# Optimization experiments

Measured on AMD Instinct MI355X. Metric: run time of the kernel, lower is better.

## Reference

```python
import jax, jax.numpy as jnp
import numpy as np

B, T, C, H, O = 64, 256, 2048, 512, 11
THRESHOLD = 1.0
LEAK = 0.003
OUTPUT_LEAK = LEAK * 0.5


def setup_inputs() -> dict:
    key = jax.random.key(0)
    k1, k2, k3, k4 = jax.random.split(key, 4)
    x = jax.random.normal(k1, (B, T, C), dtype=jnp.float32)
    # xavier_uniform(gain=0.1) for fc1: bound = 0.1*sqrt(6/(C+H))
    b1 = 0.1 * np.sqrt(6.0 / (C + H))
    w1 = jax.random.uniform(k2, (H, C), jnp.float32, -b1, b1)
    # orthogonal(gain=0.1) for fc_rec -> approximate with small gaussian scaled like orthogonal rows
    w_rec = 0.1 * jnp.linalg.qr(jax.random.normal(k3, (H, H), jnp.float32))[0]
    b2 = 0.3 * np.sqrt(6.0 / (H + O))
    w2 = jax.random.uniform(k4, (O, H), jnp.float32, -b2, b2)
    return {"x": x, "w1": w1, "w_rec": w_rec, "w2": w2}


def reference(x, w1, w_rec, w2):
    batch, t_steps, _ = x.shape
    n_hidden = w1.shape[0]
    n_output = w2.shape[0]
    dt = x.dtype

    def step(carry, x_t):
        v1, spk1, v2, out_sum = carry
        # input + recurrent current: [B,H]
        i1 = x_t @ w1.T + spk1 @ w_rec.T
        # subtractive LIF: leak, threshold, subtractive reset
        v1 = v1 + i1 - LEAK
        spk = (v1 >= THRESHOLD).astype(dt)
        v1 = v1 - spk * THRESHOLD
        # non-spiking output accumulator neuron: [B,O]
        i2 = spk @ w2.T
        v2 = jnp.maximum(v2 + i2 - OUTPUT_LEAK, 0.0)
        out_sum = out_sum + v2
        return (v1, spk, v2, out_sum), None

    init = (
        jnp.zeros((batch, n_hidden), dt),
        jnp.zeros((batch, n_hidden), dt),
        jnp.zeros((batch, n_output), dt),
        jnp.zeros((batch, n_output), dt),
    )
    (_, _, _, out_sum), _ = jax.lax.scan(step, init, jnp.swapaxes(x, 0, 1))
    return out_sum / t_steps
```

## Files before the change

kernel.cpp:

```cpp
#include <hip/hip_runtime.h>
#include <cstddef>

#define B_ 64
#define T_ 256
#define C_ 2048
#define H_ 512
#define O_ 11
#define THRESH 1.0f
#define LEAK_ 0.003f
#define OLEAK_ 0.0015f

typedef float v2f __attribute__((ext_vector_type(2)));

__global__ __launch_bounds__(256) void transpose_wrec(const float* __restrict__ w,
                                                      float* __restrict__ wt) {
    __shared__ float tile[32][33];
    int tx = threadIdx.x, ty = threadIdx.y;
    int x = blockIdx.x * 32 + tx;
    int y = blockIdx.y * 32 + ty;
#pragma unroll
    for (int i = 0; i < 32; i += 8)
        tile[ty + i][tx] = w[(size_t)(y + i) * H_ + x];
    __syncthreads();
    int x2 = blockIdx.y * 32 + tx;
    int y2 = blockIdx.x * 32 + ty;
#pragma unroll
    for (int i = 0; i < 32; i += 8)
        wt[(size_t)(y2 + i) * H_ + x2] = tile[tx][ty + i];
}

#define BM 128
#define BN 128
#define BK 16

template <int S>
__global__ __launch_bounds__(256) void gemm_ff(const float* __restrict__ A,
                                               const float* __restrict__ Bw,
                                               float* __restrict__ Pout) {
    const int K = C_;
    const int N = H_;
    const int kLen  = C_ / S;
    const int kBase = blockIdx.z * kLen;

    __shared__ float As[BK][BM];
    __shared__ float Bs[BK][BN];

    const int t  = threadIdx.x;
    const int tx = t & 15;
    const int ty = t >> 4;
    const int lr = t >> 2;
    const int lc = (t & 3) * 4;

    const float* Aptr = A  + (size_t)(blockIdx.y * BM + lr) * K + kBase + lc;
    const float* Bptr = Bw + (size_t)(blockIdx.x * BN + lr) * K + kBase + lc;

    v2f acc[8][4];
#pragma unroll
    for (int i = 0; i < 8; ++i)
#pragma unroll
        for (int j = 0; j < 4; ++j) acc[i][j] = (v2f){0.f, 0.f};

    for (int k0 = 0; k0 < kLen; k0 += BK) {
        float4 a0 = *(const float4*)(Aptr);
        float4 a1 = *(const float4*)(Aptr + (size_t)64 * K);
        float4 b0 = *(const float4*)(Bptr);
        float4 b1 = *(const float4*)(Bptr + (size_t)64 * K);
        Aptr += BK; Bptr += BK;

        __syncthreads();
        As[lc + 0][lr] = a0.x; As[lc + 1][lr] = a0.y;
        As[lc + 2][lr] = a0.z; As[lc + 3][lr] = a0.w;
        As[lc + 0][lr + 64] = a1.x; As[lc + 1][lr + 64] = a1.y;
        As[lc + 2][lr + 64] = a1.z; As[lc + 3][lr + 64] = a1.w;
        Bs[lc + 0][lr] = b0.x; Bs[lc + 1][lr] = b0.y;
        Bs[lc + 2][lr] = b0.z; Bs[lc + 3][lr] = b0.w;
        Bs[lc + 0][lr + 64] = b1.x; Bs[lc + 1][lr + 64] = b1.y;
        Bs[lc + 2][lr + 64] = b1.z; Bs[lc + 3][lr + 64] = b1.w;
        __syncthreads();

#pragma unroll
        for (int k = 0; k < BK; ++k) {
            float4 alo = *(const float4*)&As[k][ty * 4];
            float4 ahi = *(const float4*)&As[k][64 + ty * 4];
            float4 blo = *(const float4*)&Bs[k][tx * 4];
            float4 bhi = *(const float4*)&Bs[k][64 + tx * 4];
            v2f b0v = {blo.x, blo.y}, b1v = {blo.z, blo.w};
            v2f b2v = {bhi.x, bhi.y}, b3v = {bhi.z, bhi.w};
            float av[8] = {alo.x, alo.y, alo.z, alo.w, ahi.x, ahi.y, ahi.z, ahi.w};
#pragma unroll
            for (int i = 0; i < 8; ++i) {
                v2f ai = {av[i], av[i]};
                acc[i][0] += ai * b0v;
                acc[i][1] += ai * b1v;
                acc[i][2] += ai * b2v;
                acc[i][3] += ai * b3v;
            }
        }
    }

    float* P = Pout + (size_t)blockIdx.z * ((size_t)B_ * T_ * H_);
#pragma unroll
    for (int i = 0; i < 8; ++i) {
        int row = blockIdx.y * BM + (i < 4 ? ty * 4 + i : 64 + ty * 4 + (i - 4));
        float* Cp = P + (size_t)row * N + blockIdx.x * BN;
        float4 c0 = {acc[i][0].x, acc[i][0].y, acc[i][1].x, acc[i][1].y};
        float4 c1 = {acc[i][2].x, acc[i][2].y, acc[i][3].x, acc[i][3].y};
        *(float4*)(Cp + tx * 4)      = c0;
        *(float4*)(Cp + 64 + tx * 4) = c1;
    }
}

template <int S>
__global__ __launch_bounds__(512) void snn_rec(const float* __restrict__ I1,
                                               const float* __restrict__ wrT,
                                               const float* __restrict__ w2,
                                               float* __restrict__ out) {
    const int b    = blockIdx.x;
    const int h    = threadIdx.x;
    const int lane = h & 63;
    const int w    = h >> 6;

    __shared__ float w2sT[H_ * 12];
    __shared__ int   lists[2][H_];
    __shared__ int   wcnt[8];
    __shared__ float v2s[O_];
    __shared__ float osum[O_];

    for (int k = h; k < H_; k += H_) {}
#pragma unroll
    for (int o = 0; o < O_; ++o) w2sT[h * 12 + o] = w2[o * H_ + h];
    if (h < O_) { v2s[h] = 0.f; osum[h] = 0.f; }

    float v1 = 0.f;
    int   pc = 0;
    const float*  i1p  = I1 + (size_t)b * T_ * H_ + h;
    const float*  wr_h = wrT + h;
    const size_t  PARTF = (size_t)B_ * T_ * H_;

    float pf[S];
#pragma unroll
    for (int s = 0; s < S; ++s) pf[s] = i1p[s * PARTF];
    __syncthreads();

    for (int t = 0; t < T_; ++t) {
        const int cur = t & 1;

        float acc = -LEAK_;
#pragma unroll
        for (int s = 0; s < S; ++s) acc += pf[s];

        const int tn = (t + 1 < T_) ? t + 1 : t;
#pragma unroll
        for (int s = 0; s < S; ++s) pf[s] = i1p[s * PARTF + (size_t)tn * H_];

        const int* pl = lists[cur ^ 1];
        int j = 0;
        for (; j + 7 < pc; j += 8) {
            const int4 ia = *(const int4*)(pl + j);
            const int4 ib = *(const int4*)(pl + j + 4);
            float g0 = wr_h[ia.x * H_];
            float g1 = wr_h[ia.y * H_];
            float g2 = wr_h[ia.z * H_];
            float g3 = wr_h[ia.w * H_];
            float g4 = wr_h[ib.x * H_];
            float g5 = wr_h[ib.y * H_];
            float g6 = wr_h[ib.z * H_];
            float g7 = wr_h[ib.w * H_];
            acc += g0; acc += g1; acc += g2; acc += g3;
            acc += g4; acc += g5; acc += g6; acc += g7;
        }
        for (; j < pc; ++j) acc += wr_h[pl[j] * H_];

        v1 += acc;
        const bool spike = (v1 >= THRESH);
        if (spike) v1 -= THRESH;

        unsigned long long m = __ballot(spike);
        int lb = __popcll(m & ((1ull << lane) - 1ull));
        if (lane == 0) wcnt[w] = (int)__popcll(m);
        __syncthreads();

        int base = 0, tot = 0;
#pragma unroll
        for (int ww = 0; ww < 8; ++ww) {
            int c = wcnt[ww];
            if (ww < w) base += c;
            tot += c;
        }
        if (spike) lists[cur][base + lb] = h;
        __syncthreads();

        if (h < O_) {
            const int* cl = lists[cur];
            float s = 0.f;
            for (int j2 = 0; j2 < tot; ++j2) s += w2sT[cl[j2] * 12 + h];
            float v2 = v2s[h] + s - OLEAK_;
            v2 = v2 > 0.f ? v2 : 0.f;
            v2s[h] = v2;
            osum[h] += v2;
        }
        pc = tot;
    }
    __syncthreads();
    if (h < O_) out[b * O_ + h] = osum[h] * (1.0f / (float)T_);
}

extern "C" void kernel_launch(void* const* d_in, const int* in_sizes, int n_in,
                              void* d_out, int out_size, void* d_ws, size_t ws_size,
                              hipStream_t stream) {
    const float* x     = (const float*)d_in[0];
    const float* w1    = (const float*)d_in[1];
    const float* w_rec = (const float*)d_in[2];
    const float* w2    = (const float*)d_in[3];
    float* out = (float*)d_out;

    const size_t PART = (size_t)B_ * T_ * H_ * sizeof(float);
    const size_t WRT  = (size_t)H_ * H_ * sizeof(float);

    int S = 1;
    if (ws_size >= 4 * PART + WRT) S = 4;
    else if (ws_size >= 2 * PART + WRT) S = 2;

    float* P   = (float*)d_ws;
    float* wrT = (float*)((char*)d_ws + (size_t)S * PART);

    transpose_wrec<<<dim3(H_ / 32, H_ / 32), dim3(32, 8), 0, stream>>>(w_rec, wrT);

    dim3 ggrid(H_ / BN, (B_ * T_) / BM, S);
    switch (S) {
        case 4:
            gemm_ff<4><<<ggrid, dim3(256), 0, stream>>>(x, w1, P);
            snn_rec<4><<<dim3(B_), dim3(H_), 0, stream>>>(P, wrT, w2, out);
            break;
        case 2:
            gemm_ff<2><<<ggrid, dim3(256), 0, stream>>>(x, w1, P);
            snn_rec<2><<<dim3(B_), dim3(H_), 0, stream>>>(P, wrT, w2, out);
            break;
        default:
            gemm_ff<1><<<ggrid, dim3(256), 0, stream>>>(x, w1, P);
            snn_rec<1><<<dim3(B_), dim3(H_), 0, stream>>>(P, wrT, w2, out);
            break;
    }
}
```

Baseline: 764.3 us.

## Enlarge GEMM per-thread tile with register prefetch; use spike bitmasks in recurrence

The feed-forward GEMM drops to 128 threads, each computing an 8x16 output tile. Global loads for the next K-slice are issued into registers before the current slice is computed, shared tiles are padded, and results go out through nontemporal stores. The recurrent kernel replaces the prefix-sum spike list, and one of its barriers, with per-wave ballot bitmasks in shared memory. It also keeps output-neuron state in registers and double-buffers the input-current prefetch two steps ahead. The larger per-thread tile raises register pressure and can lower occupancy, and the bitmask scan turns sequential ctz walks into serial work per wave.

```diff
diff --git a/kernel.cpp b/kernel.cpp
--- a/kernel.cpp
+++ b/kernel.cpp
@@ -11,6 +11,7 @@
 #define OLEAK_ 0.0015f
 
 typedef float v2f __attribute__((ext_vector_type(2)));
+typedef float v4f __attribute__((ext_vector_type(4)));
 
 __global__ __launch_bounds__(256) void transpose_wrec(const float* __restrict__ w,
                                                       float* __restrict__ wt) {
@@ -32,81 +33,96 @@
 #define BM 128
 #define BN 128
 #define BK 16
+#define LDA (BM + 4)
+#define LDB (BN + 4)
 
 template <int S>
-__global__ __launch_bounds__(256) void gemm_ff(const float* __restrict__ A,
-                                               const float* __restrict__ Bw,
-                                               float* __restrict__ Pout) {
+__global__ __launch_bounds__(128, 2) void gemm_ff(const float* __restrict__ A,
+                                                  const float* __restrict__ Bw,
+                                                  float* __restrict__ Pout) {
     const int K = C_;
     const int N = H_;
     const int kLen  = C_ / S;
     const int kBase = blockIdx.z * kLen;
 
-    __shared__ float As[BK][BM];
-    __shared__ float Bs[BK][BN];
+    __shared__ float As[BK][LDA];
+    __shared__ float Bs[BK][LDB];
 
     const int t  = threadIdx.x;
-    const int tx = t & 15;
-    const int ty = t >> 4;
+    const int tx = t & 7;
+    const int ty = t >> 3;
     const int lr = t >> 2;
     const int lc = (t & 3) * 4;
 
-    const float* Aptr = A  + (size_t)(blockIdx.y * BM + lr) * K + kBase + lc;
-    const float* Bptr = Bw + (size_t)(blockIdx.x * BN + lr) * K + kBase + lc;
-
-    v2f acc[8][4];
+    const float* Ap = A  + (size_t)(blockIdx.y * BM + lr) * K + kBase + lc;
+    const float* Bp = Bw + (size_t)(blockIdx.x * BN + lr) * K + kBase + lc;
+
+    v2f acc[8][8];
 #pragma unroll
     for (int i = 0; i < 8; ++i)
 #pragma unroll
-        for (int j = 0; j < 4; ++j) acc[i][j] = (v2f){0.f, 0.f};
-
-    for (int k0 = 0; k0 < kLen; k0 += BK) {
-        float4 a0 = *(const float4*)(Aptr);
-        float4 a1 = *(const float4*)(Aptr + (size_t)64 * K);
-        float4 b0 = *(const float4*)(Bptr);
-        float4 b1 = *(const float4*)(Bptr + (size_t)64 * K);
-        Aptr += BK; Bptr += BK;
-
+        for (int j = 0; j < 8; ++j) acc[i][j] = (v2f){0.f, 0.f};
+
+    float4 ra[4], rb[4];
+#pragma unroll
+    for (int q = 0; q < 4; ++q) ra[q] = *(const float4*)(Ap + (size_t)(32 * q) * K);
+#pragma unroll
+    for (int q = 0; q < 4; ++q) rb[q] = *(const float4*)(Bp + (size_t)(32 * q) * K);
+
+    for (int k0 = 0;;) {
         __syncthreads();
-        As[lc + 0][lr] = a0.x; As[lc + 1][lr] = a0.y;
-        As[lc + 2][lr] = a0.z; As[lc + 3][lr] = a0.w;
-        As[lc + 0][lr + 64] = a1.x; As[lc + 1][lr + 64] = a1.y;
-        As[lc + 2][lr + 64] = a1.z; As[lc + 3][lr + 64] = a1.w;
-        Bs[lc + 0][lr] = b0.x; Bs[lc + 1][lr] = b0.y;
-        Bs[lc + 2][lr] = b0.z; Bs[lc + 3][lr] = b0.w;
-        Bs[lc + 0][lr + 64] = b1.x; Bs[lc + 1][lr + 64] = b1.y;
-        Bs[lc + 2][lr + 64] = b1.z; Bs[lc + 3][lr + 64] = b1.w;
+#pragma unroll
+        for (int q = 0; q < 4; ++q) {
+            const int r = lr + 32 * q;
+            As[lc + 0][r] = ra[q].x; As[lc + 1][r] = ra[q].y;
+            As[lc + 2][r] = ra[q].z; As[lc + 3][r] = ra[q].w;
+            Bs[lc + 0][r] = rb[q].x; Bs[lc + 1][r] = rb[q].y;
+            Bs[lc + 2][r] = rb[q].z; Bs[lc + 3][r] = rb[q].w;
+        }
         __syncthreads();
 
+        k0 += BK;
+        const bool more = (k0 < kLen);
+        if (more) {
+            Ap += BK; Bp += BK;
+#pragma unroll
+            for (int q = 0; q < 4; ++q) ra[q] = *(const float4*)(Ap + (size_t)(32 * q) * K);
+#pragma unroll
+            for (int q = 0; q < 4; ++q) rb[q] = *(const float4*)(Bp + (size_t)(32 * q) * K);
+        }
+
 #pragma unroll
         for (int k = 0; k < BK; ++k) {
-            float4 alo = *(const float4*)&As[k][ty * 4];
-            float4 ahi = *(const float4*)&As[k][64 + ty * 4];
-            float4 blo = *(const float4*)&Bs[k][tx * 4];
-            float4 bhi = *(const float4*)&Bs[k][64 + tx * 4];
-            v2f b0v = {blo.x, blo.y}, b1v = {blo.z, blo.w};
-            v2f b2v = {bhi.x, bhi.y}, b3v = {bhi.z, bhi.w};
-            float av[8] = {alo.x, alo.y, alo.z, alo.w, ahi.x, ahi.y, ahi.z, ahi.w};
+            float4 a0 = *(const float4*)&As[k][ty * 8];
+            float4 a1 = *(const float4*)&As[k][ty * 8 + 4];
+            float4 b0 = *(const float4*)&Bs[k][tx * 4];
+            float4 b1 = *(const float4*)&Bs[k][32 + tx * 4];
+            float4 b2 = *(const float4*)&Bs[k][64 + tx * 4];
+            float4 b3 = *(const float4*)&Bs[k][96 + tx * 4];
+            v2f bv[8] = {{b0.x, b0.y}, {b0.z, b0.w}, {b1.x, b1.y}, {b1.z, b1.w},
+                         {b2.x, b2.y}, {b2.z, b2.w}, {b3.x, b3.y}, {b3.z, b3.w}};
+            float av[8] = {a0.x, a0.y, a0.z, a0.w, a1.x, a1.y, a1.z, a1.w};
 #pragma unroll
             for (int i = 0; i < 8; ++i) {
                 v2f ai = {av[i], av[i]};
-                acc[i][0] += ai * b0v;
-                acc[i][1] += ai * b1v;
-                acc[i][2] += ai * b2v;
-                acc[i][3] += ai * b3v;
+#pragma unroll
+                for (int j = 0; j < 8; ++j) acc[i][j] += ai * bv[j];
             }
         }
+        if (!more) break;
     }
 
     float* P = Pout + (size_t)blockIdx.z * ((size_t)B_ * T_ * H_);
 #pragma unroll
     for (int i = 0; i < 8; ++i) {
-        int row = blockIdx.y * BM + (i < 4 ? ty * 4 + i : 64 + ty * 4 + (i - 4));
+        const int row = blockIdx.y * BM + ty * 8 + i;
         float* Cp = P + (size_t)row * N + blockIdx.x * BN;
-        float4 c0 = {acc[i][0].x, acc[i][0].y, acc[i][1].x, acc[i][1].y};
-        float4 c1 = {acc[i][2].x, acc[i][2].y, acc[i][3].x, acc[i][3].y};
-        *(float4*)(Cp + tx * 4)      = c0;
-        *(float4*)(Cp + 64 + tx * 4) = c1;
+#pragma unroll
+        for (int s = 0; s < 4; ++s) {
+            v4f c = {acc[i][2 * s].x, acc[i][2 * s].y,
+                     acc[i][2 * s + 1].x, acc[i][2 * s + 1].y};
+            __builtin_nontemporal_store(c, (v4f*)(Cp + s * 32 + tx * 4));
+        }
     }
 }
 
@@ -121,88 +137,82 @@
     const int w    = h >> 6;
 
     __shared__ float w2sT[H_ * 12];
-    __shared__ int   lists[2][H_];
-    __shared__ int   wcnt[8];
-    __shared__ float v2s[O_];
-    __shared__ float osum[O_];
-
-    for (int k = h; k < H_; k += H_) {}
+    __shared__ unsigned long long masks[2][8];
+
 #pragma unroll
     for (int o = 0; o < O_; ++o) w2sT[h * 12 + o] = w2[o * H_ + h];
-    if (h < O_) { v2s[h] = 0.f; osum[h] = 0.f; }
+    if (h < 8) { masks[0][h] = 0ull; masks[1][h] = 0ull; }
 
     float v1 = 0.f;
-    int   pc = 0;
+    float v2 = 0.f;
+    float osum = 0.f;
+
     const float*  i1p  = I1 + (size_t)b * T_ * H_ + h;
     const float*  wr_h = wrT + h;
     const size_t  PARTF = (size_t)B_ * T_ * H_;
 
-    float pf[S];
-#pragma unroll
-    for (int s = 0; s < S; ++s) pf[s] = i1p[s * PARTF];
+    float pfA[S], pfB[S];
+#pragma unroll
+    for (int s = 0; s < S; ++s) pfA[s] = __builtin_nontemporal_load(i1p + s * PARTF);
+#pragma unroll
+    for (int s = 0; s < S; ++s) pfB[s] = __builtin_nontemporal_load(i1p + s * PARTF + H_);
     __syncthreads();
 
     for (int t = 0; t < T_; ++t) {
         const int cur = t & 1;
 
         float acc = -LEAK_;
-#pragma unroll
-        for (int s = 0; s < S; ++s) acc += pf[s];
-
-        const int tn = (t + 1 < T_) ? t + 1 : t;
-#pragma unroll
-        for (int s = 0; s < S; ++s) pf[s] = i1p[s * PARTF + (size_t)tn * H_];
-
-        const int* pl = lists[cur ^ 1];
-        int j = 0;
-        for (; j + 7 < pc; j += 8) {
-            const int4 ia = *(const int4*)(pl + j);
-            const int4 ib = *(const int4*)(pl + j + 4);
-            float g0 = wr_h[ia.x * H_];
-            float g1 = wr_h[ia.y * H_];
-            float g2 = wr_h[ia.z * H_];
-            float g3 = wr_h[ia.w * H_];
-            float g4 = wr_h[ib.x * H_];
-            float g5 = wr_h[ib.y * H_];
-            float g6 = wr_h[ib.z * H_];
-            float g7 = wr_h[ib.w * H_];
-            acc += g0; acc += g1; acc += g2; acc += g3;
-            acc += g4; acc += g5; acc += g6; acc += g7;
-        }
-        for (; j < pc; ++j) acc += wr_h[pl[j] * H_];
+        if (cur == 0) {
+#pragma unroll
+            for (int s = 0; s < S; ++s) acc += pfA[s];
+            const size_t tn = (size_t)((t + 2 < T_) ? t + 2 : t);
+#pragma unroll
+            for (int s = 0; s < S; ++s)
+                pfA[s] = __builtin_nontemporal_load(i1p + s * PARTF + tn * H_);
+        } else {
+#pragma unroll
+            for (int s = 0; s < S; ++s) acc += pfB[s];
+            const size_t tn = (size_t)((t + 2 < T_) ? t + 2 : t);
+#pragma unroll
+            for (int s = 0; s < S; ++s)
+                pfB[s] = __builtin_nontemporal_load(i1p + s * PARTF + tn * H_);
+        }
+
+#pragma unroll
+        for (int ww = 0; ww < 8; ++ww) {
+            unsigned long long m = masks[cur ^ 1][ww];
+            while (m) {
+                const int idx = (ww << 6) + __builtin_ctzll(m);
+                m &= m - 1;
+                acc += wr_h[idx * H_];
+            }
+        }
 
         v1 += acc;
         const bool spike = (v1 >= THRESH);
         if (spike) v1 -= THRESH;
 
-        unsigned long long m = __ballot(spike);
-        int lb = __popcll(m & ((1ull << lane) - 1ull));
-        if (lane == 0) wcnt[w] = (int)__popcll(m);
+        const unsigned long long bm = __ballot(spike);
+        if (lane == 0) masks[cur][w] = bm;
         __syncthreads();
 
-        int base = 0, tot = 0;
-#pragma unroll
-        for (int ww = 0; ww < 8; ++ww) {
-            int c = wcnt[ww];
-            if (ww < w) base += c;
-            tot += c;
-        }
-        if (spike) lists[cur][base + lb] = h;
-        __syncthreads();
-
         if (h < O_) {
-            const int* cl = lists[cur];
-            float s = 0.f;
-            for (int j2 = 0; j2 < tot; ++j2) s += w2sT[cl[j2] * 12 + h];
-            float v2 = v2s[h] + s - OLEAK_;
-            v2 = v2 > 0.f ? v2 : 0.f;
-            v2s[h] = v2;
-            osum[h] += v2;
-        }
-        pc = tot;
-    }
-    __syncthreads();
-    if (h < O_) out[b * O_ + h] = osum[h] * (1.0f / (float)T_);
+            float s2 = 0.f;
+#pragma unroll
+            for (int ww = 0; ww < 8; ++ww) {
+                unsigned long long m = masks[cur][ww];
+                while (m) {
+                    const int idx = (ww << 6) + __builtin_ctzll(m);
+                    m &= m - 1;
+                    s2 += w2sT[idx * 12 + h];
+                }
+            }
+            float nv2 = v2 + s2 - OLEAK_;
+            v2 = nv2 > 0.f ? nv2 : 0.f;
+            osum += v2;
+        }
+    }
+    if (h < O_) out[b * O_ + h] = osum * (1.0f / (float)T_);
 }
 
 extern "C" void kernel_launch(void* const* d_in, const int* in_sizes, int n_in,
@@ -229,15 +239,15 @@
     dim3 ggrid(H_ / BN, (B_ * T_) / BM, S);
     switch (S) {
         case 4:
-            gemm_ff<4><<<ggrid, dim3(256), 0, stream>>>(x, w1, P);
+            gemm_ff<4><<<ggrid, dim3(128), 0, stream>>>(x, w1, P);
             snn_rec<4><<<dim3(B_), dim3(H_), 0, stream>>>(P, wrT, w2, out);
             break;
         case 2:
-            gemm_ff<2><<<ggrid, dim3(256), 0, stream>>>(x, w1, P);
+            gemm_ff<2><<<ggrid, dim3(128), 0, stream>>>(x, w1, P);
             snn_rec<2><<<dim3(B_), dim3(H_), 0, stream>>>(P, wrT, w2, out);
             break;
         default:
-            gemm_ff<1><<<ggrid, dim3(256), 0, stream>>>(x, w1, P);
+            gemm_ff<1><<<ggrid, dim3(128), 0, stream>>>(x, w1, P);
             snn_rec<1><<<dim3(B_), dim3(H_), 0, stream>>>(P, wrT, w2, out);
             break;
     }
```

Measured after the change: 906.1 us. 1.19x slower.

## Prefetch GEMM tiles, swizzle block order, pad LDS, deepen SNN prefetch

Applied to the files above, without the earlier changes.

The GEMM now loads the next K-tile into registers while it computes the current one, remaps block indices into an XCD-aware order, pads the LDS tiles to avoid bank conflicts, and writes outputs with nontemporal stores. The recurrent kernel prefetches input currents two steps ahead with nontemporal loads and unrolls the sparse gather over the spike list by 16. Together these aim to hide global-memory latency in both stages and to improve cache use, at the cost of more registers. The swizzle assumes the grid size is 4x128xS.

```diff
diff --git a/kernel.cpp b/kernel.cpp
--- a/kernel.cpp
+++ b/kernel.cpp
@@ -11,6 +11,7 @@
 #define OLEAK_ 0.0015f
 
 typedef float v2f __attribute__((ext_vector_type(2)));
+typedef float v4f __attribute__((ext_vector_type(4)));
 
 __global__ __launch_bounds__(256) void transpose_wrec(const float* __restrict__ w,
                                                       float* __restrict__ wt) {
@@ -32,6 +33,7 @@
 #define BM 128
 #define BN 128
 #define BK 16
+#define LDT (BM + 4)
 
 template <int S>
 __global__ __launch_bounds__(256) void gemm_ff(const float* __restrict__ A,
@@ -39,11 +41,18 @@
                                                float* __restrict__ Pout) {
     const int K = C_;
     const int N = H_;
-    const int kLen  = C_ / S;
-    const int kBase = blockIdx.z * kLen;
-
-    __shared__ float As[BK][BM];
-    __shared__ float Bs[BK][BN];
+    const int kLen = C_ / S;
+
+    const int i  = blockIdx.x + 4 * blockIdx.y + 512 * blockIdx.z;
+    const int l  = (i & 7) * (64 * S) + (i >> 3);
+    const int bx = l & 3;
+    const int by = (l >> 2) & 127;
+    const int bz = l >> 9;
+
+    const int kBase = bz * kLen;
+
+    __shared__ float As[BK][LDT];
+    __shared__ float Bs[BK][LDT];
 
     const int t  = threadIdx.x;
     const int tx = t & 15;
@@ -51,22 +60,21 @@
     const int lr = t >> 2;
     const int lc = (t & 3) * 4;
 
-    const float* Aptr = A  + (size_t)(blockIdx.y * BM + lr) * K + kBase + lc;
-    const float* Bptr = Bw + (size_t)(blockIdx.x * BN + lr) * K + kBase + lc;
+    const float* Ap = A  + (size_t)(by * BM + lr) * K + kBase + lc;
+    const float* Bp = Bw + (size_t)(bx * BN + lr) * K + kBase + lc;
 
     v2f acc[8][4];
 #pragma unroll
-    for (int i = 0; i < 8; ++i)
-#pragma unroll
-        for (int j = 0; j < 4; ++j) acc[i][j] = (v2f){0.f, 0.f};
-
-    for (int k0 = 0; k0 < kLen; k0 += BK) {
-        float4 a0 = *(const float4*)(Aptr);
-        float4 a1 = *(const float4*)(Aptr + (size_t)64 * K);
-        float4 b0 = *(const float4*)(Bptr);
-        float4 b1 = *(const float4*)(Bptr + (size_t)64 * K);
-        Aptr += BK; Bptr += BK;
-
+    for (int ii = 0; ii < 8; ++ii)
+#pragma unroll
+        for (int j = 0; j < 4; ++j) acc[ii][j] = (v2f){0.f, 0.f};
+
+    float4 a0 = *(const float4*)(Ap);
+    float4 a1 = *(const float4*)(Ap + (size_t)64 * K);
+    float4 b0 = *(const float4*)(Bp);
+    float4 b1 = *(const float4*)(Bp + (size_t)64 * K);
+
+    for (int k0 = 0;;) {
         __syncthreads();
         As[lc + 0][lr] = a0.x; As[lc + 1][lr] = a0.y;
         As[lc + 2][lr] = a0.z; As[lc + 3][lr] = a0.w;
@@ -78,6 +86,16 @@
         Bs[lc + 2][lr + 64] = b1.z; Bs[lc + 3][lr + 64] = b1.w;
         __syncthreads();
 
+        k0 += BK;
+        const bool more = (k0 < kLen);
+        if (more) {
+            Ap += BK; Bp += BK;
+            a0 = *(const float4*)(Ap);
+            a1 = *(const float4*)(Ap + (size_t)64 * K);
+            b0 = *(const float4*)(Bp);
+            b1 = *(const float4*)(Bp + (size_t)64 * K);
+        }
+
 #pragma unroll
         for (int k = 0; k < BK; ++k) {
             float4 alo = *(const float4*)&As[k][ty * 4];
@@ -88,25 +106,26 @@
             v2f b2v = {bhi.x, bhi.y}, b3v = {bhi.z, bhi.w};
             float av[8] = {alo.x, alo.y, alo.z, alo.w, ahi.x, ahi.y, ahi.z, ahi.w};
 #pragma unroll
-            for (int i = 0; i < 8; ++i) {
-                v2f ai = {av[i], av[i]};
-                acc[i][0] += ai * b0v;
-                acc[i][1] += ai * b1v;
-                acc[i][2] += ai * b2v;
-                acc[i][3] += ai * b3v;
+            for (int ii = 0; ii < 8; ++ii) {
+                v2f ai = {av[ii], av[ii]};
+                acc[ii][0] += ai * b0v;
+                acc[ii][1] += ai * b1v;
+                acc[ii][2] += ai * b2v;
+                acc[ii][3] += ai * b3v;
             }
         }
-    }
-
-    float* P = Pout + (size_t)blockIdx.z * ((size_t)B_ * T_ * H_);
-#pragma unroll
-    for (int i = 0; i < 8; ++i) {
-        int row = blockIdx.y * BM + (i < 4 ? ty * 4 + i : 64 + ty * 4 + (i - 4));
-        float* Cp = P + (size_t)row * N + blockIdx.x * BN;
-        float4 c0 = {acc[i][0].x, acc[i][0].y, acc[i][1].x, acc[i][1].y};
-        float4 c1 = {acc[i][2].x, acc[i][2].y, acc[i][3].x, acc[i][3].y};
-        *(float4*)(Cp + tx * 4)      = c0;
-        *(float4*)(Cp + 64 + tx * 4) = c1;
+        if (!more) break;
+    }
+
+    float* P = Pout + (size_t)bz * ((size_t)B_ * T_ * H_);
+#pragma unroll
+    for (int ii = 0; ii < 8; ++ii) {
+        int row = by * BM + (ii < 4 ? ty * 4 + ii : 64 + ty * 4 + (ii - 4));
+        float* Cp = P + (size_t)row * N + bx * BN;
+        v4f c0 = {acc[ii][0].x, acc[ii][0].y, acc[ii][1].x, acc[ii][1].y};
+        v4f c1 = {acc[ii][2].x, acc[ii][2].y, acc[ii][3].x, acc[ii][3].y};
+        __builtin_nontemporal_store(c0, (v4f*)(Cp + tx * 4));
+        __builtin_nontemporal_store(c1, (v4f*)(Cp + 64 + tx * 4));
     }
 }
 
@@ -126,7 +145,6 @@
     __shared__ float v2s[O_];
     __shared__ float osum[O_];
 
-    for (int k = h; k < H_; k += H_) {}
 #pragma unroll
     for (int o = 0; o < O_; ++o) w2sT[h * 12 + o] = w2[o * H_ + h];
     if (h < O_) { v2s[h] = 0.f; osum[h] = 0.f; }
@@ -137,35 +155,60 @@
     const float*  wr_h = wrT + h;
     const size_t  PARTF = (size_t)B_ * T_ * H_;
 
-    float pf[S];
-#pragma unroll
-    for (int s = 0; s < S; ++s) pf[s] = i1p[s * PARTF];
+    float pfA[S], pfB[S];
+#pragma unroll
+    for (int s = 0; s < S; ++s) pfA[s] = __builtin_nontemporal_load(i1p + s * PARTF);
+#pragma unroll
+    for (int s = 0; s < S; ++s) pfB[s] = __builtin_nontemporal_load(i1p + s * PARTF + H_);
     __syncthreads();
 
     for (int t = 0; t < T_; ++t) {
         const int cur = t & 1;
 
         float acc = -LEAK_;
-#pragma unroll
-        for (int s = 0; s < S; ++s) acc += pf[s];
-
-        const int tn = (t + 1 < T_) ? t + 1 : t;
-#pragma unroll
-        for (int s = 0; s < S; ++s) pf[s] = i1p[s * PARTF + (size_t)tn * H_];
+        if (cur == 0) {
+#pragma unroll
+            for (int s = 0; s < S; ++s) acc += pfA[s];
+            const size_t tn = (size_t)((t + 2 < T_) ? t + 2 : t);
+#pragma unroll
+            for (int s = 0; s < S; ++s)
+                pfA[s] = __builtin_nontemporal_load(i1p + s * PARTF + tn * H_);
+        } else {
+#pragma unroll
+            for (int s = 0; s < S; ++s) acc += pfB[s];
+            const size_t tn = (size_t)((t + 2 < T_) ? t + 2 : t);
+#pragma unroll
+            for (int s = 0; s < S; ++s)
+                pfB[s] = __builtin_nontemporal_load(i1p + s * PARTF + tn * H_);
+        }
 
         const int* pl = lists[cur ^ 1];
         int j = 0;
+        for (; j + 15 < pc; j += 16) {
+            const int4 ia = *(const int4*)(pl + j);
+            const int4 ib = *(const int4*)(pl + j + 4);
+            const int4 ic = *(const int4*)(pl + j + 8);
+            const int4 id = *(const int4*)(pl + j + 12);
+            float g0 = wr_h[ia.x * H_], g1 = wr_h[ia.y * H_];
+            float g2 = wr_h[ia.z * H_], g3 = wr_h[ia.w * H_];
+            float g4 = wr_h[ib.x * H_], g5 = wr_h[ib.y * H_];
+            float g6 = wr_h[ib.z * H_], g7 = wr_h[ib.w * H_];
+            float g8 = wr_h[ic.x * H_], g9 = wr_h[ic.y * H_];
+            float gA = wr_h[ic.z * H_], gB = wr_h[ic.w * H_];
+            float gC = wr_h[id.x * H_], gD = wr_h[id.y * H_];
+            float gE = wr_h[id.z * H_], gF = wr_h[id.w * H_];
+            acc += g0; acc += g1; acc += g2; acc += g3;
+            acc += g4; acc += g5; acc += g6; acc += g7;
+            acc += g8; acc += g9; acc += gA; acc += gB;
+            acc += gC; acc += gD; acc += gE; acc += gF;
+        }
         for (; j + 7 < pc; j += 8) {
             const int4 ia = *(const int4*)(pl + j);
             const int4 ib = *(const int4*)(pl + j + 4);
-            float g0 = wr_h[ia.x * H_];
-            float g1 = wr_h[ia.y * H_];
-            float g2 = wr_h[ia.z * H_];
-            float g3 = wr_h[ia.w * H_];
-            float g4 = wr_h[ib.x * H_];
-            float g5 = wr_h[ib.y * H_];
-            float g6 = wr_h[ib.z * H_];
-            float g7 = wr_h[ib.w * H_];
+            float g0 = wr_h[ia.x * H_], g1 = wr_h[ia.y * H_];
+            float g2 = wr_h[ia.z * H_], g3 = wr_h[ia.w * H_];
+            float g4 = wr_h[ib.x * H_], g5 = wr_h[ib.y * H_];
+            float g6 = wr_h[ib.z * H_], g7 = wr_h[ib.w * H_];
             acc += g0; acc += g1; acc += g2; acc += g3;
             acc += g4; acc += g5; acc += g6; acc += g7;
         }
@@ -192,9 +235,9 @@
 
         if (h < O_) {
             const int* cl = lists[cur];
-            float s = 0.f;
-            for (int j2 = 0; j2 < tot; ++j2) s += w2sT[cl[j2] * 12 + h];
-            float v2 = v2s[h] + s - OLEAK_;
+            float s2 = 0.f;
+            for (int j2 = 0; j2 < tot; ++j2) s2 += w2sT[cl[j2] * 12 + h];
+            float v2 = v2s[h] + s2 - OLEAK_;
             v2 = v2 > 0.f ? v2 : 0.f;
             v2s[h] = v2;
             osum[h] += v2;
```

Result: slower. 782.7 us (+2.4%).
